# Kernel tuning notes

Measured on AMD Instinct MI355X. Metric: run time of the kernel, lower is better.

## Reference

```python
import jax, jax.numpy as jnp
import numpy as np

N_NODES = 100000
N_EDGES = 1600000
D_IN, D_HID, D_OUT = 512, 256, 32


def setup_inputs() -> dict:
    key = jax.random.key(0)
    ks = jax.random.split(key, 8)
    features = jax.random.normal(ks[0], (N_NODES, D_IN), dtype=jnp.float32)
    A_data = jax.random.uniform(ks[1], (N_EDGES,), dtype=jnp.float32)
    A_row = jax.random.randint(ks[2], (N_EDGES,), 0, N_NODES, dtype=jnp.int32)
    A_col = jax.random.randint(ks[3], (N_EDGES,), 0, N_NODES, dtype=jnp.int32)
    # MLP params (glorot-ish scaling)
    W1 = jax.random.normal(ks[4], (D_IN, D_HID), dtype=jnp.float32) * (1.0 / np.sqrt(D_IN))
    b1 = jnp.zeros((D_HID,), dtype=jnp.float32)
    W2 = jax.random.normal(ks[5], (D_HID, D_OUT), dtype=jnp.float32) * (1.0 / np.sqrt(D_HID))
    b2 = jnp.zeros((D_OUT,), dtype=jnp.float32)
    return {"features": features, "A_data": A_data, "W1": W1, "b1": b1,
            "W2": W2, "b2": b2, "A_row": A_row, "A_col": A_col}


def reference(features, A_data, W1, b1, W2, b2, A_row, A_col):
    # head_transform: 2-layer MLP (is_training=False -> dropout identity)
    h = jax.nn.relu(features @ W1 + b1)          # [N, D_HID]
    X = h @ W2 + b2                              # [N, D_OUT]
    # propagator dropout: rate=0.0 / eval mode -> identity on A
    # sparse COO A @ X: gather columns, scale by edge values, scatter-add to rows
    msgs = A_data[:, None] * X[A_col]            # [E, D_OUT]
    out = jax.ops.segment_sum(msgs, A_row, num_segments=N_NODES)  # [N, D_OUT]
    return out
```

## Files before the change

### kernel.cpp

```cpp
#include <hip/hip_runtime.h>
#include <hip/hip_bf16.h>

typedef __bf16 bf16;
typedef __attribute__((ext_vector_type(8))) __bf16 bf16x8;
typedef __attribute__((ext_vector_type(4))) float f32x4;

constexpr int D_IN  = 512;
constexpr int D_HID = 256;
constexpr int D_OUT = 32;
constexpr int BM = 64;
constexpr int BK = 32;
constexpr int HPAD = 260;
constexpr int SCAN_VPT  = 8;
constexpr int SCAN_SPAN = 2048;

#define GLOBAL_AS(p) ((const __attribute__((address_space(1))) void*)(p))
#define LDS_AS(p)    ((__attribute__((address_space(3))) void*)(p))

__global__ __launch_bounds__(256) void prep_kernel(
    const float* __restrict__ W1, const float* __restrict__ W2,
    bf16* __restrict__ W1T, bf16* __restrict__ W2T)
{
    int idx = blockIdx.x * 256 + threadIdx.x;
    if (idx < D_IN * D_HID) {
        int k = idx / D_HID, n = idx % D_HID;
        W1T[n * D_IN + k] = (bf16)W1[idx];
    }
    int j = idx - D_IN * D_HID;
    if (j >= 0 && j < D_HID * D_OUT) {
        int k = j / D_OUT, n = j % D_OUT;
        W2T[n * D_HID + k] = (bf16)W2[j];
    }
}

__global__ __launch_bounds__(256) void fused_mlp_kernel(
    const float* __restrict__ feat,
    const bf16* __restrict__ W1T, const bf16* __restrict__ W2T,
    const float* __restrict__ b1, const float* __restrict__ b2,
    float* __restrict__ X, int N)
{
    __shared__ __align__(16) char smem[(BM + D_OUT) * HPAD * sizeof(bf16)];
    bf16* Asm  = (bf16*)smem;
    bf16* Bsm  = (bf16*)(smem + BM * BK * 2);
    bf16* Hsm  = (bf16*)smem;
    bf16* B2sm = (bf16*)(smem + BM * HPAD * 2);

    const int tid  = threadIdx.x;
    const int wave = tid >> 6;
    const int lane = tid & 63;
    const int ln   = lane & 15;
    const int q    = lane >> 4;
    const int mw   = wave * 16;
    const int r0   = blockIdx.x * BM;

    #pragma unroll
    for (int i = 0; i < 4; ++i) {
        int c  = tid + i * 256;
        int n  = c >> 5;
        int kc = (c & 31) * 8;
        *(bf16x8*)&B2sm[n * HPAD + kc] = *(const bf16x8*)&W2T[n * D_HID + kc];
    }

    f32x4 acc[16] = {};

    const int am   = tid >> 2;
    const int asub = (tid & 3) * 8;
    const long arow = (long)min(r0 + am, N - 1);
    const float* asrc = feat + arow * D_IN + asub;

    for (int k0 = 0; k0 < D_IN; k0 += BK) {
        #pragma unroll
        for (int i = 0; i < 4; ++i) {
            int c = i * 256 + wave * 64 + lane;
            const bf16* gsrc = W1T + ((c >> 2) * D_IN + k0 + (c & 3) * 8);
            bf16* lbase = Bsm + (i * 256 + wave * 64) * 8;
            __builtin_amdgcn_global_load_lds(GLOBAL_AS(gsrc), LDS_AS(lbase), 16, 0, 0);
        }

        float4 f0 = *(const float4*)(asrc + k0);
        float4 f1 = *(const float4*)(asrc + k0 + 4);
        bf16x8 av;
        av[0] = (bf16)f0.x; av[1] = (bf16)f0.y; av[2] = (bf16)f0.z; av[3] = (bf16)f0.w;
        av[4] = (bf16)f1.x; av[5] = (bf16)f1.y; av[6] = (bf16)f1.z; av[7] = (bf16)f1.w;
        *(bf16x8*)&Asm[am * BK + asub] = av;

        __syncthreads();

        bf16x8 af = *(const bf16x8*)&Asm[(mw + ln) * BK + q * 8];
        #pragma unroll
        for (int t = 0; t < 16; ++t) {
            bf16x8 bf = *(const bf16x8*)&Bsm[(t * 16 + ln) * BK + q * 8];
            acc[t] = __builtin_amdgcn_mfma_f32_16x16x32_bf16(af, bf, acc[t], 0, 0, 0);
        }
        __syncthreads();
    }

    #pragma unroll
    for (int t = 0; t < 16; ++t) {
        int colh = t * 16 + ln;
        float bb = b1[colh];
        #pragma unroll
        for (int i = 0; i < 4; ++i) {
            int row = mw + q * 4 + i;
            float v = acc[t][i] + bb;
            Hsm[row * HPAD + colh] = (bf16)fmaxf(v, 0.0f);
        }
    }
    __syncthreads();

    f32x4 acc2[2] = {};
    #pragma unroll
    for (int k0 = 0; k0 < D_HID; k0 += BK) {
        bf16x8 af = *(const bf16x8*)&Hsm[(mw + ln) * HPAD + k0 + q * 8];
        #pragma unroll
        for (int t = 0; t < 2; ++t) {
            bf16x8 bf = *(const bf16x8*)&B2sm[(t * 16 + ln) * HPAD + k0 + q * 8];
            acc2[t] = __builtin_amdgcn_mfma_f32_16x16x32_bf16(af, bf, acc2[t], 0, 0, 0);
        }
    }

    #pragma unroll
    for (int t = 0; t < 2; ++t) {
        int c = t * 16 + ln;
        float bb = b2[c];
        #pragma unroll
        for (int i = 0; i < 4; ++i) {
            int row = r0 + mw + q * 4 + i;
            if (row < N) X[row * D_OUT + c] = acc2[t][i] + bb;
        }
    }
}

__global__ __launch_bounds__(256) void hist_kernel(
    const int* __restrict__ Arow, int* __restrict__ counts, int E)
{
    int e = blockIdx.x * 256 + threadIdx.x;
    if (e < E) atomicAdd(&counts[Arow[e]], 1);
}

__global__ __launch_bounds__(256) void scanA_kernel(
    const int* __restrict__ counts, int* __restrict__ offs,
    int* __restrict__ partials, int N)
{
    __shared__ int lds[256];
    int t = threadIdx.x;
    int base = blockIdx.x * SCAN_SPAN + t * SCAN_VPT;
    int v[SCAN_VPT];
    int tsum = 0;
    #pragma unroll
    for (int j = 0; j < SCAN_VPT; ++j) {
        v[j] = (base + j < N) ? counts[base + j] : 0;
        tsum += v[j];
    }
    lds[t] = tsum;
    __syncthreads();
    for (int d = 1; d < 256; d <<= 1) {
        int x = (t >= d) ? lds[t - d] : 0;
        __syncthreads();
        lds[t] += x;
        __syncthreads();
    }
    int run = lds[t] - tsum;
    #pragma unroll
    for (int j = 0; j < SCAN_VPT; ++j) {
        if (base + j < N) offs[base + j] = run;
        run += v[j];
    }
    if (t == 255) partials[blockIdx.x] = lds[255];
}

__global__ __launch_bounds__(256) void scanB_kernel(int* __restrict__ partials, int nb)
{
    __shared__ int lds[256];
    int t = threadIdx.x;
    int v = (t < nb) ? partials[t] : 0;
    lds[t] = v;
    __syncthreads();
    for (int d = 1; d < 256; d <<= 1) {
        int x = (t >= d) ? lds[t - d] : 0;
        __syncthreads();
        lds[t] += x;
        __syncthreads();
    }
    if (t < nb) partials[t] = lds[t] - v;
}

__global__ __launch_bounds__(256) void scanC_kernel(
    int* __restrict__ offs, const int* __restrict__ partials,
    int* __restrict__ cursor, int N)
{
    int i = blockIdx.x * 256 + threadIdx.x;
    if (i < N) {
        int o = offs[i] + partials[i / SCAN_SPAN];
        offs[i] = o;
        cursor[i] = o;
    }
}

__global__ __launch_bounds__(256) void reorder_kernel(
    const int* __restrict__ Arow, const int* __restrict__ Acol,
    const float* __restrict__ Adata, int* __restrict__ cursor,
    int2* __restrict__ pairs, int E)
{
    int e = blockIdx.x * 256 + threadIdx.x;
    if (e >= E) return;
    int r = Arow[e];
    int p = atomicAdd(&cursor[r], 1);
    int2 pk;
    pk.x = Acol[e];
    pk.y = __float_as_int(Adata[e]);
    pairs[p] = pk;
}

__global__ __launch_bounds__(256) void reduce_kernel(
    const int* __restrict__ offs, const int* __restrict__ counts,
    const int2* __restrict__ pairs, const float* __restrict__ X,
    float* __restrict__ out, int N)
{
    int w    = threadIdx.x >> 6;
    int lane = threadIdx.x & 63;
    int r    = blockIdx.x * 4 + w;
    if (r >= N) return;
    int slot = lane >> 3;
    int dg   = lane & 7;
    int off  = offs[r];
    int deg  = counts[r];
    f32x4 acc = {0.0f, 0.0f, 0.0f, 0.0f};
    for (int i = slot; i < deg; i += 8) {
        int2  pk = pairs[off + i];
        float a  = __int_as_float(pk.y);
        f32x4 x  = *(const f32x4*)(X + (long)pk.x * D_OUT + dg * 4);
        acc += a * x;
    }
    #pragma unroll
    for (int d = 8; d < 64; d <<= 1) {
        acc[0] += __shfl_xor(acc[0], d, 64);
        acc[1] += __shfl_xor(acc[1], d, 64);
        acc[2] += __shfl_xor(acc[2], d, 64);
        acc[3] += __shfl_xor(acc[3], d, 64);
    }
    if (slot == 0) *(f32x4*)(out + (long)r * D_OUT + dg * 4) = acc;
}

__global__ __launch_bounds__(256) void scatter_kernel(
    const float* __restrict__ Adata, const int* __restrict__ Arow,
    const int* __restrict__ Acol, const float* __restrict__ X,
    float* __restrict__ out, int E)
{
    int idx = blockIdx.x * 256 + threadIdx.x;
    int e = idx >> 3;
    int g = idx & 7;
    if (e >= E) return;
    int   col = Acol[e];
    int   row = Arow[e];
    float a   = Adata[e];
    float4 x = *(const float4*)(X + (long)col * D_OUT + g * 4);
    float* o = out + (long)row * D_OUT + g * 4;
    unsafeAtomicAdd(o + 0, a * x.x);
    unsafeAtomicAdd(o + 1, a * x.y);
    unsafeAtomicAdd(o + 2, a * x.z);
    unsafeAtomicAdd(o + 3, a * x.w);
}

extern "C" void kernel_launch(void* const* d_in, const int* in_sizes, int n_in,
                              void* d_out, int out_size, void* d_ws, size_t ws_size,
                              hipStream_t stream)
{
    const float* feat  = (const float*)d_in[0];
    const float* Adata = (const float*)d_in[1];
    const float* W1    = (const float*)d_in[2];
    const float* b1    = (const float*)d_in[3];
    const float* W2    = (const float*)d_in[4];
    const float* b2    = (const float*)d_in[5];
    const int*   Arow  = (const int*)d_in[6];
    const int*   Acol  = (const int*)d_in[7];

    const int N = in_sizes[0] / D_IN;
    const int E = in_sizes[1];

    char* p = (char*)d_ws;
    auto alloc = [&](size_t bytes) {
        char* q = p;
        p += (bytes + 255) & ~(size_t)255;
        return q;
    };
    float* X       = (float*)alloc((size_t)N * D_OUT * sizeof(float));
    bf16*  W1T     = (bf16*) alloc((size_t)D_IN * D_HID * sizeof(bf16));
    bf16*  W2T     = (bf16*) alloc((size_t)D_HID * D_OUT * sizeof(bf16));
    int*   counts  = (int*)  alloc((size_t)N * sizeof(int));
    int*   offs    = (int*)  alloc((size_t)N * sizeof(int));
    int*   cursor  = (int*)  alloc((size_t)N * sizeof(int));
    int*   partials= (int*)  alloc(256 * sizeof(int));
    int2*  pairs   = (int2*) alloc((size_t)E * sizeof(int2));
    size_t need = (size_t)(p - (char*)d_ws);
    const bool use_csr = (need <= ws_size);

    float* out = (float*)d_out;

    int prep_elems = D_IN * D_HID + D_HID * D_OUT;
    prep_kernel<<<(prep_elems + 255) / 256, 256, 0, stream>>>(W1, W2, W1T, W2T);

    fused_mlp_kernel<<<(N + BM - 1) / BM, 256, 0, stream>>>(
        feat, W1T, W2T, b1, b2, X, N);

    if (use_csr) {
        hipMemsetAsync(counts, 0, (size_t)N * sizeof(int), stream);
        hist_kernel<<<(E + 255) / 256, 256, 0, stream>>>(Arow, counts, E);
        int nb = (N + SCAN_SPAN - 1) / SCAN_SPAN;
        scanA_kernel<<<nb, 256, 0, stream>>>(counts, offs, partials, N);
        scanB_kernel<<<1, 256, 0, stream>>>(partials, nb);
        scanC_kernel<<<(N + 255) / 256, 256, 0, stream>>>(offs, partials, cursor, N);
        reorder_kernel<<<(E + 255) / 256, 256, 0, stream>>>(
            Arow, Acol, Adata, cursor, pairs, E);
        reduce_kernel<<<(N + 3) / 4, 256, 0, stream>>>(
            offs, counts, pairs, X, out, N);
    } else {
        hipMemsetAsync(out, 0, (size_t)out_size * sizeof(float), stream);
        long scatter_threads = (long)E * 8;
        scatter_kernel<<<(scatter_threads + 255) / 256, 256, 0, stream>>>(
            Adata, Arow, Acol, X, out, E);
    }
}
```

Measured before the change: 569.1 us.

## Replace per-row CSR build with 128-row bucket sort and LDS reduction

Replaces the per-row counting sort (global histogram, three-stage scan, per-row cursor atomics) with coarse buckets of 128 rows. An LDS-privatized bucket histogram and a single-block scan replace the multi-kernel scan, and the local row index is packed into the upper bits of the column field. Each reduce block accumulates one bucket in an LDS tile using shared-memory float atomics, then writes the rows out. This cuts launches and the N-sized scan passes, and spreads the fill atomics over fewer hot counters. In exchange it adds LDS atomic contention during the reduce, and the fill now contends on only NB cursors.

```diff
diff --git a/kernel.cpp b/kernel.cpp
--- a/kernel.cpp
+++ b/kernel.cpp
@@ -11,8 +11,9 @@
 constexpr int BM = 64;
 constexpr int BK = 32;
 constexpr int HPAD = 260;
-constexpr int SCAN_VPT  = 8;
-constexpr int SCAN_SPAN = 2048;
+
+constexpr int RPB    = 128;
+constexpr int NB_MAX = 1024;
 
 #define GLOBAL_AS(p) ((const __attribute__((address_space(1))) void*)(p))
 #define LDS_AS(p)    ((__attribute__((address_space(3))) void*)(p))
@@ -89,8 +90,8 @@
         bf16x8 af = *(const bf16x8*)&Asm[(mw + ln) * BK + q * 8];
         #pragma unroll
         for (int t = 0; t < 16; ++t) {
-            bf16x8 bf = *(const bf16x8*)&Bsm[(t * 16 + ln) * BK + q * 8];
-            acc[t] = __builtin_amdgcn_mfma_f32_16x16x32_bf16(af, bf, acc[t], 0, 0, 0);
+            bf16x8 bfv = *(const bf16x8*)&Bsm[(t * 16 + ln) * BK + q * 8];
+            acc[t] = __builtin_amdgcn_mfma_f32_16x16x32_bf16(af, bfv, acc[t], 0, 0, 0);
         }
         __syncthreads();
     }
@@ -114,8 +115,8 @@
         bf16x8 af = *(const bf16x8*)&Hsm[(mw + ln) * HPAD + k0 + q * 8];
         #pragma unroll
         for (int t = 0; t < 2; ++t) {
-            bf16x8 bf = *(const bf16x8*)&B2sm[(t * 16 + ln) * HPAD + k0 + q * 8];
-            acc2[t] = __builtin_amdgcn_mfma_f32_16x16x32_bf16(af, bf, acc2[t], 0, 0, 0);
+            bf16x8 bfv = *(const bf16x8*)&B2sm[(t * 16 + ln) * HPAD + k0 + q * 8];
+            acc2[t] = __builtin_amdgcn_mfma_f32_16x16x32_bf16(af, bfv, acc2[t], 0, 0, 0);
         }
     }
 
@@ -131,28 +132,40 @@
     }
 }
 
-__global__ __launch_bounds__(256) void hist_kernel(
-    const int* __restrict__ Arow, int* __restrict__ counts, int E)
-{
-    int e = blockIdx.x * 256 + threadIdx.x;
-    if (e < E) atomicAdd(&counts[Arow[e]], 1);
-}
-
-__global__ __launch_bounds__(256) void scanA_kernel(
-    const int* __restrict__ counts, int* __restrict__ offs,
-    int* __restrict__ partials, int N)
+__global__ __launch_bounds__(256) void bhist_kernel(
+    const int* __restrict__ Arow, int* __restrict__ bcnt, int E, int NB)
+{
+    __shared__ int h[NB_MAX];
+    for (int i = threadIdx.x; i < NB; i += 256) h[i] = 0;
+    __syncthreads();
+    int base = blockIdx.x * 2048 + threadIdx.x;
+    #pragma unroll
+    for (int j = 0; j < 8; ++j) {
+        int e = base + j * 256;
+        if (e < E) atomicAdd(&h[Arow[e] >> 7], 1);
+    }
+    __syncthreads();
+    for (int i = threadIdx.x; i < NB; i += 256) {
+        int c = h[i];
+        if (c) atomicAdd(&bcnt[i], c);
+    }
+}
+
+__global__ __launch_bounds__(256) void bscan_kernel(
+    const int* __restrict__ bcnt, int* __restrict__ boffs,
+    int* __restrict__ bcur, int NB)
 {
     __shared__ int lds[256];
     int t = threadIdx.x;
-    int base = blockIdx.x * SCAN_SPAN + t * SCAN_VPT;
-    int v[SCAN_VPT];
-    int tsum = 0;
-    #pragma unroll
-    for (int j = 0; j < SCAN_VPT; ++j) {
-        v[j] = (base + j < N) ? counts[base + j] : 0;
-        tsum += v[j];
-    }
-    lds[t] = tsum;
+    int v[4];
+    int s = 0;
+    #pragma unroll
+    for (int j = 0; j < 4; ++j) {
+        int i = t * 4 + j;
+        v[j] = (i < NB) ? bcnt[i] : 0;
+        s += v[j];
+    }
+    lds[t] = s;
     __syncthreads();
     for (int d = 1; d < 256; d <<= 1) {
         int x = (t >= d) ? lds[t - d] : 0;
@@ -160,86 +173,70 @@
         lds[t] += x;
         __syncthreads();
     }
-    int run = lds[t] - tsum;
-    #pragma unroll
-    for (int j = 0; j < SCAN_VPT; ++j) {
-        if (base + j < N) offs[base + j] = run;
+    int run = lds[t] - s;
+    #pragma unroll
+    for (int j = 0; j < 4; ++j) {
+        int i = t * 4 + j;
+        if (i < NB) { boffs[i] = run; bcur[i] = run; }
         run += v[j];
     }
-    if (t == 255) partials[blockIdx.x] = lds[255];
-}
-
-__global__ __launch_bounds__(256) void scanB_kernel(int* __restrict__ partials, int nb)
-{
-    __shared__ int lds[256];
-    int t = threadIdx.x;
-    int v = (t < nb) ? partials[t] : 0;
-    lds[t] = v;
-    __syncthreads();
-    for (int d = 1; d < 256; d <<= 1) {
-        int x = (t >= d) ? lds[t - d] : 0;
-        __syncthreads();
-        lds[t] += x;
-        __syncthreads();
-    }
-    if (t < nb) partials[t] = lds[t] - v;
-}
-
-__global__ __launch_bounds__(256) void scanC_kernel(
-    int* __restrict__ offs, const int* __restrict__ partials,
-    int* __restrict__ cursor, int N)
-{
-    int i = blockIdx.x * 256 + threadIdx.x;
-    if (i < N) {
-        int o = offs[i] + partials[i / SCAN_SPAN];
-        offs[i] = o;
-        cursor[i] = o;
-    }
-}
-
-__global__ __launch_bounds__(256) void reorder_kernel(
+    if (t == 255) boffs[NB] = lds[255];
+}
+
+__global__ __launch_bounds__(256) void bfill_kernel(
     const int* __restrict__ Arow, const int* __restrict__ Acol,
-    const float* __restrict__ Adata, int* __restrict__ cursor,
-    int2* __restrict__ pairs, int E)
+    const float* __restrict__ Adata, int* __restrict__ bcur,
+    int2* __restrict__ recs, int E)
 {
     int e = blockIdx.x * 256 + threadIdx.x;
     if (e >= E) return;
     int r = Arow[e];
-    int p = atomicAdd(&cursor[r], 1);
+    int p = atomicAdd(&bcur[r >> 7], 1);
     int2 pk;
-    pk.x = Acol[e];
+    pk.x = ((r & (RPB - 1)) << 25) | Acol[e];
     pk.y = __float_as_int(Adata[e]);
-    pairs[p] = pk;
-}
-
-__global__ __launch_bounds__(256) void reduce_kernel(
-    const int* __restrict__ offs, const int* __restrict__ counts,
-    const int2* __restrict__ pairs, const float* __restrict__ X,
-    float* __restrict__ out, int N)
-{
-    int w    = threadIdx.x >> 6;
-    int lane = threadIdx.x & 63;
-    int r    = blockIdx.x * 4 + w;
-    if (r >= N) return;
-    int slot = lane >> 3;
-    int dg   = lane & 7;
-    int off  = offs[r];
-    int deg  = counts[r];
-    f32x4 acc = {0.0f, 0.0f, 0.0f, 0.0f};
-    for (int i = slot; i < deg; i += 8) {
-        int2  pk = pairs[off + i];
-        float a  = __int_as_float(pk.y);
-        f32x4 x  = *(const f32x4*)(X + (long)pk.x * D_OUT + dg * 4);
-        acc += a * x;
-    }
-    #pragma unroll
-    for (int d = 8; d < 64; d <<= 1) {
-        acc[0] += __shfl_xor(acc[0], d, 64);
-        acc[1] += __shfl_xor(acc[1], d, 64);
-        acc[2] += __shfl_xor(acc[2], d, 64);
-        acc[3] += __shfl_xor(acc[3], d, 64);
-    }
-    if (slot == 0) *(f32x4*)(out + (long)r * D_OUT + dg * 4) = acc;
+    recs[p] = pk;
+}
+
+__global__ __launch_bounds__(256) void breduce_kernel(
+    const int* __restrict__ boffs, const int2* __restrict__ recs,
+    const float* __restrict__ X, float* __restrict__ out, int N)
+{
+    __shared__ float acc[RPB * 33];
+    int t = threadIdx.x;
+    for (int i = t; i < RPB * 33; i += 256) acc[i] = 0.0f;
+    __syncthreads();
+
+    int b     = blockIdx.x;
+    int start = boffs[b];
+    int end   = boffs[b + 1];
+    int slot  = t >> 3;
+    int dg    = t & 7;
+
+    for (int i = start + slot; i < end; i += 32) {
+        int2  pk  = recs[i];
+        int   lr  = ((unsigned)pk.x) >> 25;
+        int   col = pk.x & ((1 << 25) - 1);
+        float a   = __int_as_float(pk.y);
+        f32x4 x   = *(const f32x4*)(X + (long)col * D_OUT + dg * 4);
+        float* ap = &acc[lr * 33 + dg * 4];
+        atomicAdd(ap + 0, a * x[0]);
+        atomicAdd(ap + 1, a * x[1]);
+        atomicAdd(ap + 2, a * x[2]);
+        atomicAdd(ap + 3, a * x[3]);
+    }
+    __syncthreads();
+
+    long r0 = (long)b * RPB;
+    for (int c = t; c < RPB * 8; c += 256) {
+        int row = c >> 3, g = c & 7;
+        long gr = r0 + row;
+        if (gr < N) {
+            f32x4 v = { acc[row * 33 + g * 4 + 0], acc[row * 33 + g * 4 + 1],
+                        acc[row * 33 + g * 4 + 2], acc[row * 33 + g * 4 + 3] };
+            *(f32x4*)(out + gr * D_OUT + g * 4) = v;
+        }
+    }
 }
 
 __global__ __launch_bounds__(256) void scatter_kernel(
@@ -277,6 +274,7 @@
 
     const int N = in_sizes[0] / D_IN;
     const int E = in_sizes[1];
+    const int NB = (N + RPB - 1) / RPB;
 
     char* p = (char*)d_ws;
     auto alloc = [&](size_t bytes) {
@@ -284,16 +282,15 @@
         p += (bytes + 255) & ~(size_t)255;
         return q;
     };
-    float* X       = (float*)alloc((size_t)N * D_OUT * sizeof(float));
-    bf16*  W1T     = (bf16*) alloc((size_t)D_IN * D_HID * sizeof(bf16));
-    bf16*  W2T     = (bf16*) alloc((size_t)D_HID * D_OUT * sizeof(bf16));
-    int*   counts  = (int*)  alloc((size_t)N * sizeof(int));
-    int*   offs    = (int*)  alloc((size_t)N * sizeof(int));
-    int*   cursor  = (int*)  alloc((size_t)N * sizeof(int));
-    int*   partials= (int*)  alloc(256 * sizeof(int));
-    int2*  pairs   = (int2*) alloc((size_t)E * sizeof(int2));
+    float* X     = (float*)alloc((size_t)N * D_OUT * sizeof(float));
+    bf16*  W1T   = (bf16*) alloc((size_t)D_IN * D_HID * sizeof(bf16));
+    bf16*  W2T   = (bf16*) alloc((size_t)D_HID * D_OUT * sizeof(bf16));
+    int*   bcnt  = (int*)  alloc((size_t)NB * sizeof(int));
+    int*   boffs = (int*)  alloc((size_t)(NB + 1) * sizeof(int));
+    int*   bcur  = (int*)  alloc((size_t)NB * sizeof(int));
+    int2*  recs  = (int2*) alloc((size_t)E * sizeof(int2));
     size_t need = (size_t)(p - (char*)d_ws);
-    const bool use_csr = (need <= ws_size);
+    const bool use_bucket = (need <= ws_size) && (NB <= NB_MAX) && (N <= (1 << 25));
 
     float* out = (float*)d_out;
 
@@ -303,17 +300,13 @@
     fused_mlp_kernel<<<(N + BM - 1) / BM, 256, 0, stream>>>(
         feat, W1T, W2T, b1, b2, X, N);
 
-    if (use_csr) {
-        hipMemsetAsync(counts, 0, (size_t)N * sizeof(int), stream);
-        hist_kernel<<<(E + 255) / 256, 256, 0, stream>>>(Arow, counts, E);
-        int nb = (N + SCAN_SPAN - 1) / SCAN_SPAN;
-        scanA_kernel<<<nb, 256, 0, stream>>>(counts, offs, partials, N);
-        scanB_kernel<<<1, 256, 0, stream>>>(partials, nb);
-        scanC_kernel<<<(N + 255) / 256, 256, 0, stream>>>(offs, partials, cursor, N);
-        reorder_kernel<<<(E + 255) / 256, 256, 0, stream>>>(
-            Arow, Acol, Adata, cursor, pairs, E);
-        reduce_kernel<<<(N + 3) / 4, 256, 0, stream>>>(
-            offs, counts, pairs, X, out, N);
+    if (use_bucket) {
+        hipMemsetAsync(bcnt, 0, (size_t)NB * sizeof(int), stream);
+        bhist_kernel<<<(E + 2047) / 2048, 256, 0, stream>>>(Arow, bcnt, E, NB);
+        bscan_kernel<<<1, 256, 0, stream>>>(bcnt, boffs, bcur, NB);
+        bfill_kernel<<<(E + 255) / 256, 256, 0, stream>>>(
+            Arow, Acol, Adata, bcur, recs, E);
+        breduce_kernel<<<NB, 256, 0, stream>>>(boffs, recs, X, out, N);
     } else {
         hipMemsetAsync(out, 0, (size_t)out_size * sizeof(float), stream);
         long scatter_threads = (long)E * 8;
```

New measurement: 1.080 ms. +89.7%, slower.

## Load MLP A-fragments directly to registers and slice CSR reorder by row range

Applied to the files above, without the earlier changes.

The MLP kernel now loads each lane's feature fragment straight from global memory into MFMA registers and drops the LDS staging of the A tile, which removes one LDS write/read per K step. The reorder kernel is launched with eight times as many blocks. Each block handles one row-range slice, so the atomics and scattered writes of concurrently running blocks fall into a narrower region of cursor/pairs, aiming at better locality or L2 residency. The cost is that Arow is read eight times over and most threads exit early. The uncoalesced per-lane A loads could also hurt the GEMM.

```diff
diff --git a/kernel.cpp b/kernel.cpp
--- a/kernel.cpp
+++ b/kernel.cpp
@@ -13,6 +13,7 @@
 constexpr int HPAD = 260;
 constexpr int SCAN_VPT  = 8;
 constexpr int SCAN_SPAN = 2048;
+constexpr int NSLICE = 8;
 
 #define GLOBAL_AS(p) ((const __attribute__((address_space(1))) void*)(p))
 #define LDS_AS(p)    ((__attribute__((address_space(3))) void*)(p))
@@ -40,8 +41,7 @@
     float* __restrict__ X, int N)
 {
     __shared__ __align__(16) char smem[(BM + D_OUT) * HPAD * sizeof(bf16)];
-    bf16* Asm  = (bf16*)smem;
-    bf16* Bsm  = (bf16*)(smem + BM * BK * 2);
+    bf16* Bsm  = (bf16*)smem;
     bf16* Hsm  = (bf16*)smem;
     bf16* B2sm = (bf16*)(smem + BM * HPAD * 2);
 
@@ -63,10 +63,8 @@
 
     f32x4 acc[16] = {};
 
-    const int am   = tid >> 2;
-    const int asub = (tid & 3) * 8;
-    const long arow = (long)min(r0 + am, N - 1);
-    const float* asrc = feat + arow * D_IN + asub;
+    const long arow = (long)min(r0 + mw + ln, N - 1);
+    const float* asrc = feat + arow * D_IN + q * 8;
 
     for (int k0 = 0; k0 < D_IN; k0 += BK) {
         #pragma unroll
@@ -79,18 +77,16 @@
 
         float4 f0 = *(const float4*)(asrc + k0);
         float4 f1 = *(const float4*)(asrc + k0 + 4);
-        bf16x8 av;
-        av[0] = (bf16)f0.x; av[1] = (bf16)f0.y; av[2] = (bf16)f0.z; av[3] = (bf16)f0.w;
-        av[4] = (bf16)f1.x; av[5] = (bf16)f1.y; av[6] = (bf16)f1.z; av[7] = (bf16)f1.w;
-        *(bf16x8*)&Asm[am * BK + asub] = av;
-
-        __syncthreads();
-
-        bf16x8 af = *(const bf16x8*)&Asm[(mw + ln) * BK + q * 8];
+        bf16x8 af;
+        af[0] = (bf16)f0.x; af[1] = (bf16)f0.y; af[2] = (bf16)f0.z; af[3] = (bf16)f0.w;
+        af[4] = (bf16)f1.x; af[5] = (bf16)f1.y; af[6] = (bf16)f1.z; af[7] = (bf16)f1.w;
+
+        __syncthreads();
+
         #pragma unroll
         for (int t = 0; t < 16; ++t) {
-            bf16x8 bf = *(const bf16x8*)&Bsm[(t * 16 + ln) * BK + q * 8];
-            acc[t] = __builtin_amdgcn_mfma_f32_16x16x32_bf16(af, bf, acc[t], 0, 0, 0);
+            bf16x8 bfv = *(const bf16x8*)&Bsm[(t * 16 + ln) * BK + q * 8];
+            acc[t] = __builtin_amdgcn_mfma_f32_16x16x32_bf16(af, bfv, acc[t], 0, 0, 0);
         }
         __syncthreads();
     }
@@ -111,11 +107,11 @@
     f32x4 acc2[2] = {};
     #pragma unroll
     for (int k0 = 0; k0 < D_HID; k0 += BK) {
-        bf16x8 af = *(const bf16x8*)&Hsm[(mw + ln) * HPAD + k0 + q * 8];
+        bf16x8 af2 = *(const bf16x8*)&Hsm[(mw + ln) * HPAD + k0 + q * 8];
         #pragma unroll
         for (int t = 0; t < 2; ++t) {
-            bf16x8 bf = *(const bf16x8*)&B2sm[(t * 16 + ln) * HPAD + k0 + q * 8];
-            acc2[t] = __builtin_amdgcn_mfma_f32_16x16x32_bf16(af, bf, acc2[t], 0, 0, 0);
+            bf16x8 bfv = *(const bf16x8*)&B2sm[(t * 16 + ln) * HPAD + k0 + q * 8];
+            acc2[t] = __builtin_amdgcn_mfma_f32_16x16x32_bf16(af2, bfv, acc2[t], 0, 0, 0);
         }
     }
 
@@ -200,11 +196,14 @@
 __global__ __launch_bounds__(256) void reorder_kernel(
     const int* __restrict__ Arow, const int* __restrict__ Acol,
     const float* __restrict__ Adata, int* __restrict__ cursor,
-    int2* __restrict__ pairs, int E)
-{
-    int e = blockIdx.x * 256 + threadIdx.x;
+    int2* __restrict__ pairs, int E, int rps)
+{
+    int b = blockIdx.x;
+    int slice = b & (NSLICE - 1);
+    int e = (b >> 3) * 256 + threadIdx.x;
     if (e >= E) return;
     int r = Arow[e];
+    if ((unsigned)(r - slice * rps) >= (unsigned)rps) return;
     int p = atomicAdd(&cursor[r], 1);
     int2 pk;
     pk.x = Acol[e];
@@ -310,8 +309,9 @@
         scanA_kernel<<<nb, 256, 0, stream>>>(counts, offs, partials, N);
         scanB_kernel<<<1, 256, 0, stream>>>(partials, nb);
         scanC_kernel<<<(N + 255) / 256, 256, 0, stream>>>(offs, partials, cursor, N);
-        reorder_kernel<<<(E + 255) / 256, 256, 0, stream>>>(
-            Arow, Acol, Adata, cursor, pairs, E);
+        int rps = (N + NSLICE - 1) / NSLICE;
+        reorder_kernel<<<NSLICE * ((E + 255) / 256), 256, 0, stream>>>(
+            Arow, Acol, Adata, cursor, pairs, E, rps);
         reduce_kernel<<<(N + 3) / 4, 256, 0, stream>>>(
             offs, counts, pairs, X, out, N);
     } else {
```

After: 544.7 us. 4.3% less time.
